# Kernel tuning notes

Hardware: AMD Instinct MI355X
Metric: run time of the kernel (lower is better)

The kernel has to match this reference:

```python
import jax, jax.numpy as jnp
import numpy as np

DIM = 2048
N_HEADS = 32
N_KV_HEADS = 8
HEAD_DIM = DIM // N_HEADS  # 64
N_REP = N_HEADS // N_KV_HEADS  # 4
B, S = 2, 2048
MASK_VAL = -32768.0


def setup_inputs() -> dict:
    key = jax.random.key(0)
    ks = jax.random.split(key, 7)
    x = jax.random.normal(ks[0], (B, S, DIM), dtype=jnp.float32)
    freqs_cos = jax.random.uniform(ks[1], (S, HEAD_DIM // 2), dtype=jnp.float32)
    freqs_sin = jax.random.uniform(ks[2], (S, HEAD_DIM // 2), dtype=jnp.float32)
    sc = 1.0 / np.sqrt(DIM)
    wq = jax.random.normal(ks[3], (N_HEADS * HEAD_DIM, DIM), dtype=jnp.float32) * sc
    wk = jax.random.normal(ks[4], (N_KV_HEADS * HEAD_DIM, DIM), dtype=jnp.float32) * sc
    wv = jax.random.normal(ks[5], (N_KV_HEADS * HEAD_DIM, DIM), dtype=jnp.float32) * sc
    wo = jax.random.normal(ks[6], (DIM, N_HEADS * HEAD_DIM), dtype=jnp.float32) * sc
    return {"x": x, "freqs_cos": freqs_cos, "freqs_sin": freqs_sin,
            "wq": wq, "wk": wk, "wv": wv, "wo": wo}


def _apply_rope(q, k, cos, sin):
    # q: [B,S,H,D], k: [B,S,Hkv,D]; interleaved real/imag pairs in last dim
    def rot(t):
        tr = t.reshape(t.shape[:-1] + (-1, 2))  # [..., D/2, 2]
        t_r, t_i = tr[..., 0], tr[..., 1]
        c = cos[None, :, None, :]  # broadcast over batch and heads
        s = sin[None, :, None, :]
        o_r = t_r * c - t_i * s
        o_i = t_r * s + t_i * c
        return jnp.stack([o_r, o_i], axis=-1).reshape(t.shape)
    return rot(q), rot(k)


def reference(x, freqs_cos, freqs_sin, wq, wk, wv, wo):
    bsz, seqlen, _ = x.shape
    xq = (x @ wq.T).reshape(bsz, seqlen, N_HEADS, HEAD_DIM)
    xk = (x @ wk.T).reshape(bsz, seqlen, N_KV_HEADS, HEAD_DIM)
    xv = (x @ wv.T).reshape(bsz, seqlen, N_KV_HEADS, HEAD_DIM)
    xq, xk = _apply_rope(xq, xk, freqs_cos, freqs_sin)
    # GQA: repeat each kv head n_rep times contiguously (matches per-head cat loop)
    xk = jnp.repeat(xk, N_REP, axis=2)  # [B,S,H,D]
    xv = jnp.repeat(xv, N_REP, axis=2)
    # [B,H,S,D]
    q = xq.transpose(0, 2, 1, 3)
    k = xk.transpose(0, 2, 1, 3)
    v = xv.transpose(0, 2, 1, 3)
    scores = jnp.einsum('bhqd,bhkd->bhqk', q, k) / jnp.sqrt(jnp.float32(HEAD_DIM))
    causal = jnp.triu(jnp.full((seqlen, seqlen), MASK_VAL, dtype=scores.dtype), k=1)
    scores = scores + causal[None, None, :, :]
    probs = jax.nn.softmax(scores.astype(jnp.float32), axis=-1).astype(q.dtype)
    out = jnp.einsum('bhqk,bhkd->bhqd', probs, v)
    out = out.transpose(0, 2, 1, 3).reshape(bsz, seqlen, -1)
    return out @ wo.T
```

## Files before the change

### kernel.cpp

```cpp
#include <hip/hip_runtime.h>
#include <hip/hip_bf16.h>
#include <type_traits>

typedef __bf16 bf16;
typedef __bf16 bf16x2 __attribute__((ext_vector_type(2)));
typedef __bf16 bf16x4 __attribute__((ext_vector_type(4)));
typedef __bf16 bf16x8 __attribute__((ext_vector_type(8)));
typedef float f32x4 __attribute__((ext_vector_type(4)));

#define AS1 __attribute__((address_space(1)))
#define AS3 __attribute__((address_space(3)))

#define KAPPA 0.180336880111f

__device__ __forceinline__ void load_lds16(const void* g, void* l) {
  __builtin_amdgcn_global_load_lds((AS1 void*)g, (AS3 void*)l, 16, 0, 0);
}
__device__ __forceinline__ float exp2_fast(float x) {
  return __builtin_amdgcn_exp2f(x);
}

__global__ void f2b_all(const float* __restrict__ x, const float* __restrict__ wq,
                        const float* __restrict__ wk, const float* __restrict__ wv,
                        const float* __restrict__ wo, bf16* __restrict__ xb,
                        bf16* __restrict__ wqkv, bf16* __restrict__ wob) {
  int bid = blockIdx.x;
  const float* src;
  bf16* dst;
  int off;
  if (bid < 8192) { src = x; dst = xb; off = bid; }
  else if (bid < 12288) { src = wq; dst = wqkv; off = bid - 8192; }
  else if (bid < 13312) { src = wk; dst = wqkv + 4194304; off = bid - 12288; }
  else if (bid < 14336) { src = wv; dst = wqkv + 5242880; off = bid - 13312; }
  else { src = wo; dst = wob; off = bid - 14336; }
  int i = (off * 256 + threadIdx.x) * 4;
  float4 v = *(const float4*)(src + i);
  bf16x4 o = {(bf16)v.x, (bf16)v.y, (bf16)v.z, (bf16)v.w};
  *(bf16x4*)(dst + i) = o;
}

__global__ __launch_bounds__(512, 2) void gemm_qkv(const bf16* __restrict__ A,
                                                   const bf16* __restrict__ Bw,
                                                   const float* __restrict__ fc,
                                                   const float* __restrict__ fs,
                                                   bf16* __restrict__ Qro,
                                                   bf16* __restrict__ Kro,
                                                   bf16* __restrict__ Vt) {
  const int K = 2048;
  __shared__ bf16 As[4][256][32];
  __shared__ bf16 Bs[4][256][32];
  const int t = threadIdx.x;
  const int wave = t >> 6, lane = t & 63, qd = lane >> 4, ln = lane & 15;
  const int wm = (wave >> 2) * 128;
  const int wn = (wave & 3) * 64;
  const int bn = blockIdx.x;
  const int bmrow = blockIdx.y * 256;

  const bf16* Ab = A + (size_t)bmrow * K;
  const bf16* Bb = Bw + (size_t)bn * 256 * K;

  auto stage1 = [&](const bf16* gb, char* lb, int tk, int sub) {
    int e = sub * 512 + t;
    int ro = e >> 2, gs = (e & 3) ^ ((ro >> 1) & 3);
    load_lds16(gb + (size_t)ro * K + tk * 32 + gs * 8,
               lb + (tk & 3) * 16384 + sub * 8192 + wave * 1024);
  };

#pragma unroll
  for (int tt = 0; tt < 3; tt++) {
    stage1(Ab, (char*)As, tt, 0);
    stage1(Ab, (char*)As, tt, 1);
    stage1(Bb, (char*)Bs, tt, 0);
    stage1(Bb, (char*)Bs, tt, 1);
  }
  asm volatile("s_waitcnt vmcnt(8)" ::: "memory");
  __builtin_amdgcn_s_barrier();

  f32x4 acc[8][4] = {};
  bf16x8 bfr[4];
  const int segoff = (qd ^ ((ln >> 1) & 3)) << 4;

  for (int tk = 0; tk < 64; tk++) {
    const char* Asl = (const char*)As + (tk & 3) * 16384;
    const char* Bsl = (const char*)Bs + (tk & 3) * 16384;

    bf16x8 af[4];
#pragma unroll
    for (int i = 0; i < 4; i++)
      af[i] = *(const bf16x8*)(Asl + (wm + i * 16 + ln) * 64 + segoff);
#pragma unroll
    for (int j = 0; j < 4; j++)
      bfr[j] = *(const bf16x8*)(Bsl + (wn + j * 16 + ln) * 64 + segoff);
    if (tk + 3 < 64) {
      stage1(Ab, (char*)As, tk + 3, 0);
      stage1(Ab, (char*)As, tk + 3, 1);
    }
    __builtin_amdgcn_s_barrier();
    asm volatile("s_waitcnt lgkmcnt(0)" ::: "memory");
    __builtin_amdgcn_sched_barrier(0);
    __builtin_amdgcn_s_setprio(1);
#pragma unroll
    for (int i = 0; i < 4; i++)
#pragma unroll
      for (int j = 0; j < 4; j++)
        acc[i][j] = __builtin_amdgcn_mfma_f32_16x16x32_bf16(af[i], bfr[j],
                                                            acc[i][j], 0, 0, 0);
    __builtin_amdgcn_s_setprio(0);
    __builtin_amdgcn_s_barrier();

#pragma unroll
    for (int i = 0; i < 4; i++)
      af[i] = *(const bf16x8*)(Asl + (wm + 64 + i * 16 + ln) * 64 + segoff);
    if (tk + 3 < 64) {
      stage1(Bb, (char*)Bs, tk + 3, 0);
      stage1(Bb, (char*)Bs, tk + 3, 1);
    }
    if (tk < 61) asm volatile("s_waitcnt vmcnt(8)" ::: "memory");
    else if (tk == 61) asm volatile("s_waitcnt vmcnt(4)" ::: "memory");
    else asm volatile("s_waitcnt vmcnt(0)" ::: "memory");
    __builtin_amdgcn_s_barrier();
    asm volatile("s_waitcnt lgkmcnt(0)" ::: "memory");
    __builtin_amdgcn_sched_barrier(0);
    __builtin_amdgcn_s_setprio(1);
#pragma unroll
    for (int i = 0; i < 4; i++)
#pragma unroll
      for (int j = 0; j < 4; j++)
        acc[4 + i][j] = __builtin_amdgcn_mfma_f32_16x16x32_bf16(
            af[i], bfr[j], acc[4 + i][j], 0, 0, 0);
    __builtin_amdgcn_s_setprio(0);
    __builtin_amdgcn_s_barrier();
  }

  const int b = bmrow >> 11;
  const int sb = (bmrow & 2047) + wm;
  const bool odd = ln & 1;

  if (bn < 10) {
    const bool isQ = bn < 8;
    const float kap = isQ ? KAPPA : 1.0f;
    const int h = (isQ ? bn : bn - 8) * 4 + (wave & 3);
    bf16* dst = isQ ? (Qro + (size_t)(b * 32 + h) * 2048 * 64)
                    : (Kro + (size_t)(b * 8 + h) * 2048 * 64);
#pragma unroll
    for (int i = 0; i < 8; i++) {
#pragma unroll
      for (int j = 0; j < 4; j++) {
        const int d = j * 16 + ln;
        const int i_f = d >> 1;
#pragma unroll
        for (int r = 0; r < 4; r++) {
          int s = sb + i * 16 + qd * 4 + r;
          float v = acc[i][j][r];
          float p = __shfl_xor(v, 1);
          float cv = fc[s * 32 + i_f] * kap;
          float sv = fs[s * 32 + i_f] * kap;
          float o = odd ? (p * sv + v * cv) : (v * cv - p * sv);
          dst[(size_t)s * 64 + d] = (bf16)o;
        }
      }
    }
  } else {
    const int kh = (bn - 10) * 4 + (wave & 3);
#pragma unroll
    for (int i = 0; i < 8; i++)
#pragma unroll
      for (int j = 0; j < 4; j++) {
        const int d = j * 16 + ln;
        int s = sb + i * 16 + qd * 4;
        bf16x4 ov = {(bf16)acc[i][j][0], (bf16)acc[i][j][1],
                     (bf16)acc[i][j][2], (bf16)acc[i][j][3]};
        *(bf16x4*)&Vt[((size_t)(b * 8 + kh) * 64 + d) * 2048 + s] = ov;
      }
  }
}

template <typename OutT>
__global__ __launch_bounds__(256, 4) void gemm_bt64(const bf16* __restrict__ A,
                                                    const bf16* __restrict__ Bw,
                                                    OutT* __restrict__ C,
                                                    int M, int N, int K) {
  __shared__ bf16 As[64][64];
  __shared__ bf16 Bs[128][64];
  const int t = threadIdx.x;
  const int wave = t >> 6, lane = t & 63, qd = lane >> 4, ln = lane & 15;
  const int wm = (wave >> 1) * 32;
  const int wn = (wave & 1) * 64;
  const size_t bm = (size_t)blockIdx.y * 64;
  const size_t bn = (size_t)blockIdx.x * 128;

  const bf16* Ab = A + bm * (size_t)K;
  const bf16* Bb = Bw + bn * (size_t)K;

  f32x4 acc[2][4] = {};

  for (int k0 = 0; k0 < K; k0 += 64) {
#pragma unroll
    for (int i = 0; i < 2; i++) {
      int e = i * 256 + t;
      int ro = e >> 3, gs = (e & 7) ^ (ro & 7);
      load_lds16(Ab + (size_t)ro * K + k0 + gs * 8,
                 (char*)As + i * 4096 + wave * 1024);
    }
#pragma unroll
    for (int i = 0; i < 4; i++) {
      int e = i * 256 + t;
      int ro = e >> 3, gs = (e & 7) ^ (ro & 7);
      load_lds16(Bb + (size_t)ro * K + k0 + gs * 8,
                 (char*)Bs + i * 4096 + wave * 1024);
    }
    __syncthreads();

#pragma unroll
    for (int kk = 0; kk < 2; kk++) {
      bf16x8 af[2], bfr[4];
#pragma unroll
      for (int i = 0; i < 2; i++) {
        int row = wm + i * 16 + ln;
        int ps = (kk * 4 + qd) ^ (row & 7);
        af[i] = *(const bf16x8*)((const char*)As + row * 128 + ps * 16);
      }
#pragma unroll
      for (int j = 0; j < 4; j++) {
        int row = wn + j * 16 + ln;
        int ps = (kk * 4 + qd) ^ (row & 7);
        bfr[j] = *(const bf16x8*)((const char*)Bs + row * 128 + ps * 16);
      }
#pragma unroll
      for (int i = 0; i < 2; i++)
#pragma unroll
        for (int j = 0; j < 4; j++)
          acc[i][j] = __builtin_amdgcn_mfma_f32_16x16x32_bf16(af[i], bfr[j],
                                                              acc[i][j], 0, 0, 0);
    }
    __syncthreads();
  }

#pragma unroll
  for (int i = 0; i < 2; i++)
#pragma unroll
    for (int j = 0; j < 4; j++)
#pragma unroll
      for (int r = 0; r < 4; r++) {
        size_t row = bm + wm + i * 16 + qd * 4 + r;
        size_t col = bn + wn + j * 16 + ln;
        C[row * N + col] = (OutT)acc[i][j][r];
      }
}

__global__ __launch_bounds__(256, 3) void attn_fwd(const bf16* __restrict__ Q,
                                                   const bf16* __restrict__ Kg,
                                                   const bf16* __restrict__ Vg,
                                                   bf16* __restrict__ O) {
  __shared__ bf16 Ks[2][64][64];
  __shared__ bf16 Vs[2][64][64];
  __shared__ bf16 Ps[128][64];
  const int t = threadIdx.x;
  const int wave = t >> 6, lane = t & 63, qd = lane >> 4, ln = lane & 15;
  const int bid = blockIdx.x;
  const int qt = 15 - (bid >> 6);
  const int bh = bid & 63;
  const int b = bh >> 5, h = bh & 31, kh = h >> 2;
  const bf16* Qb = Q + ((size_t)(b * 32 + h) * 2048 + qt * 128) * 64;
  const bf16* Kb = Kg + (size_t)(b * 8 + kh) * 2048 * 64;
  const bf16* Vb = Vg + (size_t)(b * 8 + kh) * 64 * 2048;
  char* PsB = (char*)Ps;

  bf16x8 qf[2][2];
#pragma unroll
  for (int kk = 0; kk < 2; kk++)
#pragma unroll
    for (int mi = 0; mi < 2; mi++)
      qf[kk][mi] = *(const bf16x8*)(Qb + (wave * 32 + mi * 16 + ln) * 64 +
                                    (kk * 4 + qd) * 8);

  auto stageKV = [&](int kb, int buf) {
#pragma unroll
    for (int i = 0; i < 2; i++) {
      int e = i * 256 + t;
      int row = e >> 3, sg = (e & 7) ^ (row & 7);
      load_lds16(Kb + (size_t)(kb * 64 + row) * 64 + sg * 8,
                 (char*)Ks + buf * 8192 + i * 4096 + wave * 1024);
      load_lds16(Vb + (size_t)row * 2048 + kb * 64 + sg * 8,
                 (char*)Vs + buf * 8192 + i * 4096 + wave * 1024);
    }
  };

  f32x4 o_acc[4][2] = {};
  float l_st[2] = {0.f, 0.f};
  const int q0 = qt * 128 + wave * 32;
  const int nkb = 2 * qt + 2;

  stageKV(0, 0);
  __syncthreads();

  for (int kb = 0; kb < nkb; kb++) {
    const int cur = kb & 1;
    if (kb + 1 < nkb) stageKV(kb + 1, cur ^ 1);
    const char* Ksl = (const char*)Ks + cur * 8192;
    const char* Vsl = (const char*)Vs + cur * 8192;

    f32x4 s_acc[4][2] = {};
#pragma unroll
    for (int kk = 0; kk < 2; kk++) {
      bf16x8 ak[4];
#pragma unroll
      for (int j = 0; j < 4; j++) {
        int row = j * 16 + ln;
        int ph = (kk * 4 + qd) ^ (ln & 7);
        ak[j] = *(const bf16x8*)(Ksl + row * 128 + ph * 16);
      }
#pragma unroll
      for (int j = 0; j < 4; j++)
#pragma unroll
        for (int mi = 0; mi < 2; mi++)
          s_acc[j][mi] = __builtin_amdgcn_mfma_f32_16x16x32_bf16(
              ak[j], qf[kk][mi], s_acc[j][mi], 0, 0, 0);
    }

    auto smax = [&](auto maskc) {
      constexpr bool MASK = decltype(maskc)::value;
#pragma unroll
      for (int mi = 0; mi < 2; mi++) {
        const int qv = q0 + mi * 16 + ln;
        const int prow = wave * 32 + mi * 16 + ln;
        float rs = 0.f;
#pragma unroll
        for (int j = 0; j < 4; j++) {
          bf16x4 pk;
#pragma unroll
          for (int r = 0; r < 4; r++) {
            float s = s_acc[j][mi][r];
            if (MASK) {
              int k_glob = kb * 64 + j * 16 + qd * 4 + r;
              if (k_glob > qv) s = -1e5f;
            }
            float pv = exp2_fast(s - 16.f);
            rs += pv;
            pk[r] = (bf16)pv;
          }
          int ps = (j * 2 + (qd >> 1)) ^ (ln & 7);
          *(bf16x4*)(PsB + prow * 128 + ps * 16 + (qd & 1) * 8) = pk;
        }
        l_st[mi] += rs;
      }
    };
    if (kb * 64 + 63 > q0) smax(std::true_type{});
    else smax(std::false_type{});

#pragma unroll
    for (int kk = 0; kk < 2; kk++) {
      bf16x8 av[4], bp[2];
#pragma unroll
      for (int dj = 0; dj < 4; dj++) {
        int row = dj * 16 + ln;
        int ph = (kk * 4 + qd) ^ (ln & 7);
        av[dj] = *(const bf16x8*)(Vsl + row * 128 + ph * 16);
      }
#pragma unroll
      for (int mi = 0; mi < 2; mi++) {
        int prow = wave * 32 + mi * 16 + ln;
        int ph = (kk * 4 + qd) ^ (ln & 7);
        bp[mi] = *(const bf16x8*)(PsB + prow * 128 + ph * 16);
      }
#pragma unroll
      for (int dj = 0; dj < 4; dj++)
#pragma unroll
        for (int mi = 0; mi < 2; mi++)
          o_acc[dj][mi] = __builtin_amdgcn_mfma_f32_16x16x32_bf16(
              av[dj], bp[mi], o_acc[dj][mi], 0, 0, 0);
    }

    __syncthreads();
  }

#pragma unroll
  for (int mi = 0; mi < 2; mi++) {
    float lt = l_st[mi];
    lt += __shfl_xor(lt, 16);
    lt += __shfl_xor(lt, 32);
    float inv = 1.f / lt;
    int q_idx = qt * 128 + wave * 32 + mi * 16 + ln;
#pragma unroll
    for (int dj = 0; dj < 4; dj++) {
      bf16x4 ov;
#pragma unroll
      for (int r = 0; r < 4; r++) ov[r] = (bf16)(o_acc[dj][mi][r] * inv);
      *(bf16x4*)&O[((size_t)(b * 2048 + q_idx) * 32 + h) * 64 + dj * 16 + qd * 4] = ov;
    }
  }
}

extern "C" void kernel_launch(void* const* d_in, const int* in_sizes, int n_in,
                              void* d_out, int out_size, void* d_ws,
                              size_t ws_size, hipStream_t stream) {
  const float* x = (const float*)d_in[0];
  const float* fc = (const float*)d_in[1];
  const float* fs = (const float*)d_in[2];
  const float* wq = (const float*)d_in[3];
  const float* wk = (const float*)d_in[4];
  const float* wv = (const float*)d_in[5];
  const float* wo = (const float*)d_in[6];
  float* out = (float*)d_out;

  char* ws = (char*)d_ws;
  const size_t MB = (size_t)1 << 20;
  bf16* xb   = (bf16*)(ws + 0 * MB);
  bf16* wqkv = (bf16*)(ws + 16 * MB);
  bf16* wob  = (bf16*)(ws + 28 * MB);
  bf16* Qro  = (bf16*)(ws + 36 * MB);
  bf16* Kro  = (bf16*)(ws + 52 * MB);
  bf16* Vt   = (bf16*)(ws + 56 * MB);
  bf16* Oa   = (bf16*)(ws + 60 * MB);

  dim3 blk(256);
  f2b_all<<<18432, blk, 0, stream>>>(x, wq, wk, wv, wo, xb, wqkv, wob);
  gemm_qkv<<<dim3(12, 16), dim3(512), 0, stream>>>(xb, wqkv, fc, fs, Qro, Kro, Vt);
  attn_fwd<<<1024, blk, 0, stream>>>(Qro, Kro, Vt, Oa);
  gemm_bt64<float><<<dim3(16, 64), blk, 0, stream>>>(Oa, wob, out, 4096, 2048, 2048);
}
```

Baseline: 275.1 us.

## Retile QKV and output GEMMs to 128x128 blocks with triple-buffered LDS pipeline

Result: slower. 282.3 us (+2.6%).

```diff
diff --git a/kernel.cpp b/kernel.cpp
--- a/kernel.cpp
+++ b/kernel.cpp
@@ -39,7 +39,7 @@
   *(bf16x4*)(dst + i) = o;
 }
 
-__global__ __launch_bounds__(512, 2) void gemm_qkv(const bf16* __restrict__ A,
+__global__ __launch_bounds__(256, 3) void gemm_qkv(const bf16* __restrict__ A,
                                                    const bf16* __restrict__ Bw,
                                                    const float* __restrict__ fc,
                                                    const float* __restrict__ fs,
@@ -47,55 +47,55 @@
                                                    bf16* __restrict__ Kro,
                                                    bf16* __restrict__ Vt) {
   const int K = 2048;
-  __shared__ bf16 As[4][256][32];
-  __shared__ bf16 Bs[4][256][32];
+  __shared__ bf16 As[3][128][32];
+  __shared__ bf16 Bs[3][128][32];
   const int t = threadIdx.x;
   const int wave = t >> 6, lane = t & 63, qd = lane >> 4, ln = lane & 15;
-  const int wm = (wave >> 2) * 128;
-  const int wn = (wave & 3) * 64;
+  const int wm = (wave >> 1) * 64;
+  const int wn = (wave & 1) * 64;
   const int bn = blockIdx.x;
-  const int bmrow = blockIdx.y * 256;
-
-  const bf16* Ab = A + (size_t)bmrow * K;
-  const bf16* Bb = Bw + (size_t)bn * 256 * K;
-
-  auto stage1 = [&](const bf16* gb, char* lb, int tk, int sub) {
-    int e = sub * 512 + t;
-    int ro = e >> 2, gs = (e & 3) ^ ((ro >> 1) & 3);
-    load_lds16(gb + (size_t)ro * K + tk * 32 + gs * 8,
-               lb + (tk & 3) * 16384 + sub * 8192 + wave * 1024);
+  const size_t bm = (size_t)blockIdx.y * 128;
+
+  const bf16* Ab = A + bm * (size_t)K;
+  const bf16* Bb = Bw + (size_t)bn * 128 * K;
+
+  auto stage = [&](const bf16* gb, char* lb, int tk, int slot) {
+#pragma unroll
+    for (int sub = 0; sub < 2; sub++) {
+      int e = sub * 256 + t;
+      int ro = e >> 2, gs = (e & 3) ^ ((ro >> 1) & 3);
+      load_lds16(gb + (size_t)ro * K + tk * 32 + gs * 8,
+                 lb + slot * 8192 + sub * 4096 + wave * 1024);
+    }
   };
 
-#pragma unroll
-  for (int tt = 0; tt < 3; tt++) {
-    stage1(Ab, (char*)As, tt, 0);
-    stage1(Ab, (char*)As, tt, 1);
-    stage1(Bb, (char*)Bs, tt, 0);
-    stage1(Bb, (char*)Bs, tt, 1);
-  }
-  asm volatile("s_waitcnt vmcnt(8)" ::: "memory");
+  stage(Ab, (char*)As, 0, 0);
+  stage(Bb, (char*)Bs, 0, 0);
+  stage(Ab, (char*)As, 1, 1);
+  stage(Bb, (char*)Bs, 1, 1);
+  asm volatile("s_waitcnt vmcnt(4)" ::: "memory");
   __builtin_amdgcn_s_barrier();
 
-  f32x4 acc[8][4] = {};
-  bf16x8 bfr[4];
+  f32x4 acc[4][4] = {};
   const int segoff = (qd ^ ((ln >> 1) & 3)) << 4;
 
+  int cs = 0, ps = 2;
   for (int tk = 0; tk < 64; tk++) {
-    const char* Asl = (const char*)As + (tk & 3) * 16384;
-    const char* Bsl = (const char*)Bs + (tk & 3) * 16384;
-
-    bf16x8 af[4];
+    if (tk < 62) {
+      stage(Ab, (char*)As, tk + 2, ps);
+      stage(Bb, (char*)Bs, tk + 2, ps);
+    }
+    const char* Asl = (const char*)As + cs * 8192;
+    const char* Bsl = (const char*)Bs + cs * 8192;
+
+    bf16x8 af[4], bfr[4];
 #pragma unroll
     for (int i = 0; i < 4; i++)
       af[i] = *(const bf16x8*)(Asl + (wm + i * 16 + ln) * 64 + segoff);
 #pragma unroll
     for (int j = 0; j < 4; j++)
       bfr[j] = *(const bf16x8*)(Bsl + (wn + j * 16 + ln) * 64 + segoff);
-    if (tk + 3 < 64) {
-      stage1(Ab, (char*)As, tk + 3, 0);
-      stage1(Ab, (char*)As, tk + 3, 1);
-    }
-    __builtin_amdgcn_s_barrier();
+
     asm volatile("s_waitcnt lgkmcnt(0)" ::: "memory");
     __builtin_amdgcn_sched_barrier(0);
     __builtin_amdgcn_s_setprio(1);
@@ -106,44 +106,26 @@
         acc[i][j] = __builtin_amdgcn_mfma_f32_16x16x32_bf16(af[i], bfr[j],
                                                             acc[i][j], 0, 0, 0);
     __builtin_amdgcn_s_setprio(0);
+
+    if (tk < 62) asm volatile("s_waitcnt vmcnt(4)" ::: "memory");
+    else if (tk == 62) asm volatile("s_waitcnt vmcnt(0)" ::: "memory");
     __builtin_amdgcn_s_barrier();
-
-#pragma unroll
-    for (int i = 0; i < 4; i++)
-      af[i] = *(const bf16x8*)(Asl + (wm + 64 + i * 16 + ln) * 64 + segoff);
-    if (tk + 3 < 64) {
-      stage1(Bb, (char*)Bs, tk + 3, 0);
-      stage1(Bb, (char*)Bs, tk + 3, 1);
-    }
-    if (tk < 61) asm volatile("s_waitcnt vmcnt(8)" ::: "memory");
-    else if (tk == 61) asm volatile("s_waitcnt vmcnt(4)" ::: "memory");
-    else asm volatile("s_waitcnt vmcnt(0)" ::: "memory");
-    __builtin_amdgcn_s_barrier();
-    asm volatile("s_waitcnt lgkmcnt(0)" ::: "memory");
-    __builtin_amdgcn_sched_barrier(0);
-    __builtin_amdgcn_s_setprio(1);
-#pragma unroll
-    for (int i = 0; i < 4; i++)
-#pragma unroll
-      for (int j = 0; j < 4; j++)
-        acc[4 + i][j] = __builtin_amdgcn_mfma_f32_16x16x32_bf16(
-            af[i], bfr[j], acc[4 + i][j], 0, 0, 0);
-    __builtin_amdgcn_s_setprio(0);
-    __builtin_amdgcn_s_barrier();
+    cs = (cs == 2) ? 0 : cs + 1;
+    ps = (ps == 2) ? 0 : ps + 1;
   }
 
-  const int b = bmrow >> 11;
-  const int sb = (bmrow & 2047) + wm;
+  const int b = (int)(bm >> 11);
+  const int sb = (int)(bm & 2047) + wm;
   const bool odd = ln & 1;
 
-  if (bn < 10) {
-    const bool isQ = bn < 8;
+  if (bn < 20) {
+    const bool isQ = bn < 16;
     const float kap = isQ ? KAPPA : 1.0f;
-    const int h = (isQ ? bn : bn - 8) * 4 + (wave & 3);
-    bf16* dst = isQ ? (Qro + (size_t)(b * 32 + h) * 2048 * 64)
-                    : (Kro + (size_t)(b * 8 + h) * 2048 * 64);
-#pragma unroll
-    for (int i = 0; i < 8; i++) {
+    const int hh = isQ ? (bn * 2 + (wn >> 6)) : ((bn - 16) * 2 + (wn >> 6));
+    bf16* dst = isQ ? (Qro + ((size_t)(b * 32 + hh) * 2048) * 64)
+                    : (Kro + ((size_t)(b * 8 + hh) * 2048) * 64);
+#pragma unroll
+    for (int i = 0; i < 4; i++) {
 #pragma unroll
       for (int j = 0; j < 4; j++) {
         const int d = j * 16 + ln;
@@ -161,9 +143,9 @@
       }
     }
   } else {
-    const int kh = (bn - 10) * 4 + (wave & 3);
-#pragma unroll
-    for (int i = 0; i < 8; i++)
+    const int kh = (bn - 20) * 2 + (wn >> 6);
+#pragma unroll
+    for (int i = 0; i < 4; i++)
 #pragma unroll
       for (int j = 0; j < 4; j++) {
         const int d = j * 16 + ln;
@@ -175,76 +157,86 @@
   }
 }
 
-template <typename OutT>
-__global__ __launch_bounds__(256, 4) void gemm_bt64(const bf16* __restrict__ A,
-                                                    const bf16* __restrict__ Bw,
-                                                    OutT* __restrict__ C,
-                                                    int M, int N, int K) {
-  __shared__ bf16 As[64][64];
-  __shared__ bf16 Bs[128][64];
+__global__ __launch_bounds__(256, 2) void gemm_bt(const bf16* __restrict__ A,
+                                                  const bf16* __restrict__ Bw,
+                                                  float* __restrict__ C) {
+  const int K = 2048, N = 2048;
+  __shared__ bf16 As[3][128][32];
+  __shared__ bf16 Bs[3][128][32];
   const int t = threadIdx.x;
   const int wave = t >> 6, lane = t & 63, qd = lane >> 4, ln = lane & 15;
-  const int wm = (wave >> 1) * 32;
+  const int wm = (wave >> 1) * 64;
   const int wn = (wave & 1) * 64;
-  const size_t bm = (size_t)blockIdx.y * 64;
+  const size_t bm = (size_t)blockIdx.y * 128;
   const size_t bn = (size_t)blockIdx.x * 128;
 
   const bf16* Ab = A + bm * (size_t)K;
   const bf16* Bb = Bw + bn * (size_t)K;
 
-  f32x4 acc[2][4] = {};
-
-  for (int k0 = 0; k0 < K; k0 += 64) {
-#pragma unroll
-    for (int i = 0; i < 2; i++) {
-      int e = i * 256 + t;
-      int ro = e >> 3, gs = (e & 7) ^ (ro & 7);
-      load_lds16(Ab + (size_t)ro * K + k0 + gs * 8,
-                 (char*)As + i * 4096 + wave * 1024);
-    }
-#pragma unroll
-    for (int i = 0; i < 4; i++) {
-      int e = i * 256 + t;
-      int ro = e >> 3, gs = (e & 7) ^ (ro & 7);
-      load_lds16(Bb + (size_t)ro * K + k0 + gs * 8,
-                 (char*)Bs + i * 4096 + wave * 1024);
-    }
-    __syncthreads();
-
-#pragma unroll
-    for (int kk = 0; kk < 2; kk++) {
-      bf16x8 af[2], bfr[4];
-#pragma unroll
-      for (int i = 0; i < 2; i++) {
-        int row = wm + i * 16 + ln;
-        int ps = (kk * 4 + qd) ^ (row & 7);
-        af[i] = *(const bf16x8*)((const char*)As + row * 128 + ps * 16);
-      }
-#pragma unroll
-      for (int j = 0; j < 4; j++) {
-        int row = wn + j * 16 + ln;
-        int ps = (kk * 4 + qd) ^ (row & 7);
-        bfr[j] = *(const bf16x8*)((const char*)Bs + row * 128 + ps * 16);
-      }
-#pragma unroll
-      for (int i = 0; i < 2; i++)
-#pragma unroll
-        for (int j = 0; j < 4; j++)
-          acc[i][j] = __builtin_amdgcn_mfma_f32_16x16x32_bf16(af[i], bfr[j],
-                                                              acc[i][j], 0, 0, 0);
-    }
-    __syncthreads();
+  auto stage = [&](const bf16* gb, char* lb, int tk, int slot) {
+#pragma unroll
+    for (int sub = 0; sub < 2; sub++) {
+      int e = sub * 256 + t;
+      int ro = e >> 2, gs = (e & 3) ^ ((ro >> 1) & 3);
+      load_lds16(gb + (size_t)ro * K + tk * 32 + gs * 8,
+                 lb + slot * 8192 + sub * 4096 + wave * 1024);
+    }
+  };
+
+  stage(Ab, (char*)As, 0, 0);
+  stage(Bb, (char*)Bs, 0, 0);
+  stage(Ab, (char*)As, 1, 1);
+  stage(Bb, (char*)Bs, 1, 1);
+  asm volatile("s_waitcnt vmcnt(4)" ::: "memory");
+  __builtin_amdgcn_s_barrier();
+
+  f32x4 acc[4][4] = {};
+  const int segoff = (qd ^ ((ln >> 1) & 3)) << 4;
+
+  int cs = 0, ps = 2;
+  for (int tk = 0; tk < 64; tk++) {
+    if (tk < 62) {
+      stage(Ab, (char*)As, tk + 2, ps);
+      stage(Bb, (char*)Bs, tk + 2, ps);
+    }
+    const char* Asl = (const char*)As + cs * 8192;
+    const char* Bsl = (const char*)Bs + cs * 8192;
+
+    bf16x8 af[4], bfr[4];
+#pragma unroll
+    for (int i = 0; i < 4; i++)
+      af[i] = *(const bf16x8*)(Asl + (wm + i * 16 + ln) * 64 + segoff);
+#pragma unroll
+    for (int j = 0; j < 4; j++)
+      bfr[j] = *(const bf16x8*)(Bsl + (wn + j * 16 + ln) * 64 + segoff);
+
+    asm volatile("s_waitcnt lgkmcnt(0)" ::: "memory");
+    __builtin_amdgcn_sched_barrier(0);
+    __builtin_amdgcn_s_setprio(1);
+#pragma unroll
+    for (int i = 0; i < 4; i++)
+#pragma unroll
+      for (int j = 0; j < 4; j++)
+        acc[i][j] = __builtin_amdgcn_mfma_f32_16x16x32_bf16(af[i], bfr[j],
+                                                            acc[i][j], 0, 0, 0);
+    __builtin_amdgcn_s_setprio(0);
+
+    if (tk < 62) asm volatile("s_waitcnt vmcnt(4)" ::: "memory");
+    else if (tk == 62) asm volatile("s_waitcnt vmcnt(0)" ::: "memory");
+    __builtin_amdgcn_s_barrier();
+    cs = (cs == 2) ? 0 : cs + 1;
+    ps = (ps == 2) ? 0 : ps + 1;
   }
 
 #pragma unroll
-  for (int i = 0; i < 2; i++)
+  for (int i = 0; i < 4; i++)
 #pragma unroll
     for (int j = 0; j < 4; j++)
 #pragma unroll
       for (int r = 0; r < 4; r++) {
         size_t row = bm + wm + i * 16 + qd * 4 + r;
         size_t col = bn + wn + j * 16 + ln;
-        C[row * N + col] = (OutT)acc[i][j][r];
+        C[row * N + col] = acc[i][j][r];
       }
 }
 
@@ -415,7 +407,7 @@
 
   dim3 blk(256);
   f2b_all<<<18432, blk, 0, stream>>>(x, wq, wk, wv, wo, xb, wqkv, wob);
-  gemm_qkv<<<dim3(12, 16), dim3(512), 0, stream>>>(xb, wqkv, fc, fs, Qro, Kro, Vt);
+  gemm_qkv<<<dim3(24, 32), blk, 0, stream>>>(xb, wqkv, fc, fs, Qro, Kro, Vt);
   attn_fwd<<<1024, blk, 0, stream>>>(Qro, Kro, Vt, Oa);
-  gemm_bt64<float><<<dim3(16, 64), blk, 0, stream>>>(Oa, wob, out, 4096, 2048, 2048);
-}
+  gemm_bt<<<dim3(16, 32), blk, 0, stream>>>(Oa, wob, out);
+}
```
